# Kernel optimization log

Hardware: AMD Instinct MI355X
Metric: run time of the kernel (lower is better)

Reference implementation:

```python
import jax, jax.numpy as jnp
import numpy as np

B, T, C, H = 8, 2048, 1024, 64


def setup_inputs() -> dict:
    key = jax.random.key(0)
    k1, k2, k3, k4 = jax.random.split(key, 4)
    data = jax.random.normal(k1, (B, T, C), dtype=jnp.float32)
    # nn.Linear(embed, head, bias=False) weights, stored as [embed, head] so y = x @ W
    scale = C ** -0.5  # init-scale so activations stay O(1)
    Wq = jax.random.normal(k2, (C, H), dtype=jnp.float32) * scale
    Wk = jax.random.normal(k3, (C, H), dtype=jnp.float32) * scale
    Wv = jax.random.normal(k4, (C, H), dtype=jnp.float32) * scale
    return {"data": data, "Wq": Wq, "Wk": Wk, "Wv": Wv}


def reference(data, Wq, Wk, Wv):
    # data: [B, T, C]; self-attention (crossData=None), causal mask, eval-mode dropout.
    Bs, Ts, Cs = data.shape
    q = data @ Wq  # [B, T, H]
    k = data @ Wk  # [B, T, H]
    v = data @ Wv  # [B, T, H]
    # NOTE: original scales by C**-0.5 with C = embed_size (faithful to source).
    wei = jnp.einsum('btd,bsd->bts', q, k) * (Cs ** -0.5)  # [B, T, T]
    causal = jnp.tril(jnp.ones((Ts, Ts), dtype=bool))
    wei = jnp.where(causal[None, :, :], wei, -jnp.inf)
    wei = jax.nn.softmax(wei, axis=-1)
    out = jnp.einsum('bts,bsh->bth', wei, v)  # [B, T, H]
    return out
```

## Files before the change

### kernel.cpp

```cpp
#include <hip/hip_runtime.h>
#include <hip/hip_bf16.h>


typedef __bf16 bf16;
typedef __bf16 bf16x8 __attribute__((ext_vector_type(8)));
typedef float f32x4 __attribute__((ext_vector_type(4)));
typedef unsigned int u32;
typedef u32 u32x2 __attribute__((ext_vector_type(2)));
typedef u32 u32x4 __attribute__((ext_vector_type(4)));

#define T_SZ 2048
#define C_SZ 1024
#define H_SZ 64
#define QOFF 0
#define KOFF 1024
#define VOFF 2048
#define PPITCH 72
#define APITCH 1032
#define NEG_BIG (-30000.0f)
#define QSCALE 0.04508422f

__device__ __forceinline__ bf16x8 ld8(const bf16* p) { return *(const bf16x8*)p; }

template <int CTRL>
__device__ __forceinline__ float dpp_mov(float x) {
  return __builtin_bit_cast(float,
      __builtin_amdgcn_update_dpp(0, __builtin_bit_cast(int, x), CTRL, 0xf, 0xf, true));
}
__device__ __forceinline__ float qmax16(float x) {
  x = fmaxf(x, dpp_mov<0x121>(x));
  x = fmaxf(x, dpp_mov<0x122>(x));
  x = fmaxf(x, dpp_mov<0x124>(x));
  x = fmaxf(x, dpp_mov<0x128>(x));
  return x;
}
__device__ __forceinline__ float qsum16(float x) {
  x += dpp_mov<0x121>(x);
  x += dpp_mov<0x122>(x);
  x += dpp_mov<0x124>(x);
  x += dpp_mov<0x128>(x);
  return x;
}

__global__ __launch_bounds__(256) void transpose_w(const float* __restrict__ Wq,
                                                   const float* __restrict__ Wk,
                                                   const float* __restrict__ Wv,
                                                   bf16* __restrict__ Wt) {
  __shared__ float sh[64][65];
  int ct = blockIdx.x;
  int mat = blockIdx.y;
  const float* W = (mat == 0) ? Wq : (mat == 1 ? Wk : Wv);
  int tid = threadIdx.x;
  int r = tid >> 2, cb = (tid & 3) * 16;

  const f32x4* src = (const f32x4*)(W + (size_t)(ct * 64 + r) * H_SZ + cb);
#pragma unroll
  for (int v = 0; v < 4; ++v) {
    f32x4 x = src[v];
#pragma unroll
    for (int j = 0; j < 4; ++j) sh[r][cb + v * 4 + j] = x[j];
  }
  __syncthreads();

  float scale = (mat == 0) ? QSCALE : 1.0f;
  bf16x8 o0, o1;
#pragma unroll
  for (int j = 0; j < 8; ++j) o0[j] = (bf16)(sh[cb + j][r] * scale);
#pragma unroll
  for (int j = 0; j < 8; ++j) o1[j] = (bf16)(sh[cb + 8 + j][r] * scale);
  bf16* dst = Wt + ((size_t)mat * H_SZ + r) * C_SZ + ct * 64 + cb;
  *(bf16x8*)dst = o0;
  *(bf16x8*)(dst + 8) = o1;
}

__global__ __launch_bounds__(768, 3) void qkv(const float* data, const bf16* __restrict__ Wt,
                                              bf16* arena, int regsz) {
  __shared__ bf16 As[64 * 1024];
  char* As_b = (char*)As;
  int blk = blockIdx.x;
  int tid = threadIdx.x;
  int w = tid >> 6, lane = tid & 63;
  int l15 = lane & 15, quad = lane >> 4;

  const float* src = data + (size_t)blk * 64 * C_SZ;
#pragma unroll
  for (int g = 0; g < 3; ++g) {
    f32x4 st[7];
#pragma unroll
    for (int i = 0; i < 7; ++i) {
      int u = (g * 7 + i) * 768 + tid;
      st[i] = __builtin_nontemporal_load(
          (const f32x4*)(src + (size_t)(u >> 8) * C_SZ + (u & 255) * 4));
    }
#pragma unroll
    for (int i = 0; i < 7; ++i) {
      int u = (g * 7 + i) * 768 + tid;
      int row = u >> 8, c4 = u & 255;
      bf16 t4[4] = {(bf16)st[i][0], (bf16)st[i][1], (bf16)st[i][2], (bf16)st[i][3]};
      int bo = (row * 2048 + c4 * 8) ^ ((row & 7) << 4);
      *(u32x2*)(As_b + bo) = *(const u32x2*)t4;
    }
  }
  if (tid < 256) {
    int c4 = tid;
    f32x4 x = __builtin_nontemporal_load(
        (const f32x4*)(src + (size_t)63 * C_SZ + c4 * 4));
    bf16 t4[4] = {(bf16)x[0], (bf16)x[1], (bf16)x[2], (bf16)x[3]};
    int bo = (63 * 2048 + c4 * 8) ^ ((63 & 7) << 4);
    *(u32x2*)(As_b + bo) = *(const u32x2*)t4;
  }
  __syncthreads();

  int j = w;
  const bf16* wb = Wt + (size_t)(j * 16 + l15) * C_SZ + quad * 8;
  bf16x8 wf[2];
  wf[0] = ld8(wb);
  wf[1] = ld8(wb + 32);

  f32x4 acc[4];
  f32x4 zero = {0.f, 0.f, 0.f, 0.f};
#pragma unroll
  for (int rg = 0; rg < 4; ++rg) acc[rg] = zero;

  bool isQK = (j < 8);
  int swz = (l15 & 7) << 4;

#pragma unroll 2
  for (int kci = 0; kci < 32; ++kci) {
    int cur = kci & 1;
    bf16x8 df[4];
#pragma unroll
    for (int rg = 0; rg < 4; ++rg) {
      int bo = ((rg * 16 + l15) * 2048 + kci * 64 + quad * 16) ^ swz;
      df[rg] = ld8((const bf16*)(As_b + bo));
    }
    if (isQK) {
#pragma unroll
      for (int rg = 0; rg < 4; ++rg)
        acc[rg] = __builtin_amdgcn_mfma_f32_16x16x32_bf16(wf[cur], df[rg], acc[rg], 0, 0, 0);
    } else {
#pragma unroll
      for (int rg = 0; rg < 4; ++rg)
        acc[rg] = __builtin_amdgcn_mfma_f32_16x16x32_bf16(df[rg], wf[cur], acc[rg], 0, 0, 0);
    }
    wf[cur] = ld8(wb + ((kci + 2) & 31) * 32);
  }

#pragma unroll
  for (int rg = 0; rg < 4; ++rg) {
    bf16* reg = arena + (size_t)(blk * 4 + rg) * (size_t)regsz;
    bf16 p4[4] = {(bf16)acc[rg][0], (bf16)acc[rg][1], (bf16)acc[rg][2], (bf16)acc[rg][3]};
    if (j < 4) {
      bf16* dst = reg + QOFF + l15 * 64 + j * 16 + quad * 4;
      *(u32x2*)dst = *(const u32x2*)p4;
    } else if (j < 8) {
      bf16* dst = reg + KOFF + l15 * 64 + (j - 4) * 16 + quad * 4;
      *(u32x2*)dst = *(const u32x2*)p4;
    } else {
      bf16* dst = reg + VOFF + ((j - 8) * 16 + l15) * 16 + quad * 4;
      *(u32x2*)dst = *(const u32x2*)p4;
    }
  }
}

__global__ __launch_bounds__(256, 4) void attn(const bf16* __restrict__ arena,
                                               float* __restrict__ out, int regsz) {
  __shared__ bf16 Ps[4][16 * PPITCH];
  __shared__ f32x4 Mg[3][6][64];
  int id = blockIdx.x;
  int b = id & 7;
  int t = id >> 3;
  int slice = t & 3;
  int qt = 31 - (t >> 2);
  int tid = threadIdx.x;
  int w = tid >> 6, lane = tid & 63;
  int l15 = lane & 15, quad = lane >> 4;

  const bf16* base = arena + (size_t)b * 128 * (size_t)regsz;

  const bf16* qreg = base + (size_t)(qt * 4 + slice) * (size_t)regsz + QOFF + l15 * 64;
  bf16x8 qf0 = ld8(qreg + quad * 8);
  bf16x8 qf1 = ld8(qreg + 32 + quad * 8);

  f32x4 accO[4];
  f32x4 zero = {0.f, 0.f, 0.f, 0.f};
#pragma unroll
  for (int nt = 0; nt < 4; ++nt) accO[nt] = zero;
  float m[4], l[4];
#pragma unroll
  for (int r = 0; r < 4; ++r) { m[r] = NEG_BIG; l[r] = 0.f; }

  int qrow_base = qt * 64 + slice * 16 + quad * 4;
  int vro = (quad >> 1);
  int vco = (quad & 1) * 8;

  int q4 = (qt + 4) >> 2;
  int kbeg = w * q4;
  int kend = min((w + 1) * q4, qt + 1);

  for (int kt = kbeg; kt < kend; ++kt) {
    bf16x8 kf[8];
#pragma unroll
    for (int nt = 0; nt < 4; ++nt) {
      const bf16* kp = base + (size_t)(kt * 4 + nt) * (size_t)regsz + KOFF + l15 * 64 + quad * 8;
      kf[2 * nt] = ld8(kp);
      kf[2 * nt + 1] = ld8(kp + 32);
    }

    f32x4 sA[4];
#pragma unroll
    for (int nt = 0; nt < 4; ++nt) sA[nt] = zero;
#pragma unroll
    for (int nt = 0; nt < 4; ++nt) {
      sA[nt] = __builtin_amdgcn_mfma_f32_16x16x32_bf16(qf0, kf[2 * nt], sA[nt], 0, 0, 0);
      sA[nt] = __builtin_amdgcn_mfma_f32_16x16x32_bf16(qf1, kf[2 * nt + 1], sA[nt], 0, 0, 0);
    }

    bf16x8 vf0[4];
#pragma unroll
    for (int nt = 0; nt < 4; ++nt) {
      const bf16* vp = base + (size_t)(kt * 4 + vro) * (size_t)regsz + VOFF +
                       (nt * 16 + l15) * 16 + vco;
      vf0[nt] = ld8(vp);
    }

    if (kt == qt) {
#pragma unroll
      for (int nt = 0; nt < 4; ++nt) {
        int colg = kt * 64 + nt * 16 + l15;
#pragma unroll
        for (int r = 0; r < 4; ++r)
          if (colg > qrow_base + r) sA[nt][r] = NEG_BIG;
      }
    }

    float alpha[4];
#pragma unroll
    for (int r = 0; r < 4; ++r) {
      float mx = qmax16(fmaxf(fmaxf(sA[0][r], sA[1][r]), fmaxf(sA[2][r], sA[3][r])));
      float mnew = fmaxf(m[r], mx);
      alpha[r] = exp2f(m[r] - mnew);
      m[r] = mnew;
    }

    float rs[4] = {0.f, 0.f, 0.f, 0.f};
#pragma unroll
    for (int nt = 0; nt < 4; ++nt) {
#pragma unroll
      for (int r = 0; r < 4; ++r) {
        float p = exp2f(sA[nt][r] - m[r]);
        sA[nt][r] = p;
        rs[r] += p;
      }
    }
#pragma unroll
    for (int r = 0; r < 4; ++r) l[r] = l[r] * alpha[r] + qsum16(rs[r]);

#pragma unroll
    for (int nt = 0; nt < 4; ++nt) {
#pragma unroll
      for (int r = 0; r < 4; ++r)
        Ps[w][(quad * 4 + r) * PPITCH + nt * 16 + l15] = (bf16)sA[nt][r];
    }

    bf16x8 vf1[4];
#pragma unroll
    for (int nt = 0; nt < 4; ++nt) {
      const bf16* vp = base + (size_t)(kt * 4 + 2 + vro) * (size_t)regsz + VOFF +
                       (nt * 16 + l15) * 16 + vco;
      vf1[nt] = ld8(vp);
    }

#pragma unroll
    for (int nt = 0; nt < 4; ++nt) {
#pragma unroll
      for (int r = 0; r < 4; ++r) accO[nt][r] *= alpha[r];
    }
    bf16x8 pf0 = ld8((const bf16*)Ps[w] + l15 * PPITCH + quad * 8);
    bf16x8 pf1 = ld8((const bf16*)Ps[w] + l15 * PPITCH + 32 + quad * 8);
#pragma unroll
    for (int nt = 0; nt < 4; ++nt)
      accO[nt] = __builtin_amdgcn_mfma_f32_16x16x32_bf16(pf0, vf0[nt], accO[nt], 0, 0, 0);
#pragma unroll
    for (int nt = 0; nt < 4; ++nt)
      accO[nt] = __builtin_amdgcn_mfma_f32_16x16x32_bf16(pf1, vf1[nt], accO[nt], 0, 0, 0);
  }

  if (w > 0) {
#pragma unroll
    for (int nt = 0; nt < 4; ++nt) Mg[w - 1][nt][lane] = accO[nt];
    f32x4 mv = {m[0], m[1], m[2], m[3]};
    f32x4 lv = {l[0], l[1], l[2], l[3]};
    Mg[w - 1][4][lane] = mv;
    Mg[w - 1][5][lane] = lv;
  }
  __syncthreads();
  if (w == 0) {
#pragma unroll
    for (int wv = 0; wv < 3; ++wv) {
      f32x4 mo = Mg[wv][4][lane];
      f32x4 lo = Mg[wv][5][lane];
      f32x4 oo[4];
#pragma unroll
      for (int nt = 0; nt < 4; ++nt) oo[nt] = Mg[wv][nt][lane];
#pragma unroll
      for (int r = 0; r < 4; ++r) {
        float mnew = fmaxf(m[r], mo[r]);
        float a = exp2f(m[r] - mnew);
        float bs = exp2f(mo[r] - mnew);
        l[r] = l[r] * a + lo[r] * bs;
#pragma unroll
        for (int nt = 0; nt < 4; ++nt) accO[nt][r] = accO[nt][r] * a + oo[nt][r] * bs;
        m[r] = mnew;
      }
    }

    float inv[4];
#pragma unroll
    for (int r = 0; r < 4; ++r) inv[r] = 1.f / l[r];
#pragma unroll
    for (int nt = 0; nt < 4; ++nt) {
#pragma unroll
      for (int r = 0; r < 4; ++r) {
        int tk = qt * 64 + slice * 16 + quad * 4 + r;
        int h = nt * 16 + l15;
        out[((size_t)b * T_SZ + tk) * H_SZ + h] = accO[nt][r] * inv[r];
      }
    }
  }
}

extern "C" void kernel_launch(void* const* d_in, const int* in_sizes, int n_in,
                              void* d_out, int out_size, void* d_ws, size_t ws_size,
                              hipStream_t stream) {
  const float* data = (const float*)d_in[0];

  const size_t arena_bytes = (size_t)1024 * 4096 * sizeof(bf16);
  const size_t wt_bytes = (size_t)3 * H_SZ * C_SZ * sizeof(bf16);
  bool ws_ok = (d_ws != nullptr) && (ws_size >= arena_bytes + wt_bytes);

  bf16* arena = ws_ok ? (bf16*)d_ws : (bf16*)d_in[0];
  bf16* Wt = ws_ok ? (bf16*)((char*)d_ws + arena_bytes) : (bf16*)d_out;
  int regsz = ws_ok ? 4096 : 32768;

  transpose_w<<<dim3(16, 3), 256, 0, stream>>>((const float*)d_in[1],
                                               (const float*)d_in[2],
                                               (const float*)d_in[3], Wt);
  qkv<<<256, 768, 0, stream>>>(data, Wt, arena, regsz);
  attn<<<1024, 256, 0, stream>>>(arena, (float*)d_out, regsz);
}
```

Before: 143.2 us.

## Split QKV projection into two row halves to overlap global loads with MFMA

The qkv kernel now stages the 64-row data tile in two halves of 32 rows. Global loads for the second half are issued into registers before the MFMA loop over the first half, then converted and written to shared memory afterwards. The aim is to hide part of the global-load latency of the fp32 input behind compute. In exchange it holds more live registers (st2 is 11 x f32x4), which risks spills or lower occupancy under launch bounds of 768 threads and 3 blocks. It also streams the weight fragments twice, once per half.

Result: slower. 154.1 us (+7.6%).

```diff
diff --git a/kernel.cpp b/kernel.cpp
--- a/kernel.cpp
+++ b/kernel.cpp
@@ -16,7 +16,6 @@
 #define KOFF 1024
 #define VOFF 2048
 #define PPITCH 72
-#define APITCH 1032
 #define NEG_BIG (-30000.0f)
 #define QSCALE 0.04508422f
 
@@ -83,33 +82,40 @@
   int l15 = lane & 15, quad = lane >> 4;
 
   const float* src = data + (size_t)blk * 64 * C_SZ;
-#pragma unroll
-  for (int g = 0; g < 3; ++g) {
-    f32x4 st[7];
-#pragma unroll
-    for (int i = 0; i < 7; ++i) {
-      int u = (g * 7 + i) * 768 + tid;
-      st[i] = __builtin_nontemporal_load(
+
+  {
+    f32x4 st[11];
+#pragma unroll
+    for (int i = 0; i < 11; ++i) {
+      if (i < 10 || tid < 512) {
+        int u = i * 768 + tid;
+        st[i] = __builtin_nontemporal_load(
+            (const f32x4*)(src + (size_t)(u >> 8) * C_SZ + (u & 255) * 4));
+      }
+    }
+#pragma unroll
+    for (int i = 0; i < 11; ++i) {
+      if (i < 10 || tid < 512) {
+        int u = i * 768 + tid;
+        int row = u >> 8, c4 = u & 255;
+        bf16 t4[4] = {(bf16)st[i][0], (bf16)st[i][1], (bf16)st[i][2], (bf16)st[i][3]};
+        int bo = (row * 2048 + c4 * 8) ^ ((row & 7) << 4);
+        *(u32x2*)(As_b + bo) = *(const u32x2*)t4;
+      }
+    }
+  }
+  __syncthreads();
+
+  f32x4 st2[11];
+#pragma unroll
+  for (int i = 0; i < 11; ++i) {
+    if (i < 10 || tid < 512) {
+      int u = 8192 + i * 768 + tid;
+      st2[i] = __builtin_nontemporal_load(
           (const f32x4*)(src + (size_t)(u >> 8) * C_SZ + (u & 255) * 4));
     }
-#pragma unroll
-    for (int i = 0; i < 7; ++i) {
-      int u = (g * 7 + i) * 768 + tid;
-      int row = u >> 8, c4 = u & 255;
-      bf16 t4[4] = {(bf16)st[i][0], (bf16)st[i][1], (bf16)st[i][2], (bf16)st[i][3]};
-      int bo = (row * 2048 + c4 * 8) ^ ((row & 7) << 4);
-      *(u32x2*)(As_b + bo) = *(const u32x2*)t4;
-    }
-  }
-  if (tid < 256) {
-    int c4 = tid;
-    f32x4 x = __builtin_nontemporal_load(
-        (const f32x4*)(src + (size_t)63 * C_SZ + c4 * 4));
-    bf16 t4[4] = {(bf16)x[0], (bf16)x[1], (bf16)x[2], (bf16)x[3]};
-    int bo = (63 * 2048 + c4 * 8) ^ ((63 & 7) << 4);
-    *(u32x2*)(As_b + bo) = *(const u32x2*)t4;
-  }
-  __syncthreads();
+  }
+  __builtin_amdgcn_sched_barrier(0);
 
   int j = w;
   const bf16* wb = Wt + (size_t)(j * 16 + l15) * C_SZ + quad * 8;
@@ -128,20 +134,49 @@
 #pragma unroll 2
   for (int kci = 0; kci < 32; ++kci) {
     int cur = kci & 1;
-    bf16x8 df[4];
-#pragma unroll
-    for (int rg = 0; rg < 4; ++rg) {
+    bf16x8 df[2];
+#pragma unroll
+    for (int rg = 0; rg < 2; ++rg) {
       int bo = ((rg * 16 + l15) * 2048 + kci * 64 + quad * 16) ^ swz;
       df[rg] = ld8((const bf16*)(As_b + bo));
     }
     if (isQK) {
-#pragma unroll
-      for (int rg = 0; rg < 4; ++rg)
-        acc[rg] = __builtin_amdgcn_mfma_f32_16x16x32_bf16(wf[cur], df[rg], acc[rg], 0, 0, 0);
+      acc[0] = __builtin_amdgcn_mfma_f32_16x16x32_bf16(wf[cur], df[0], acc[0], 0, 0, 0);
+      acc[1] = __builtin_amdgcn_mfma_f32_16x16x32_bf16(wf[cur], df[1], acc[1], 0, 0, 0);
     } else {
-#pragma unroll
-      for (int rg = 0; rg < 4; ++rg)
-        acc[rg] = __builtin_amdgcn_mfma_f32_16x16x32_bf16(df[rg], wf[cur], acc[rg], 0, 0, 0);
+      acc[0] = __builtin_amdgcn_mfma_f32_16x16x32_bf16(df[0], wf[cur], acc[0], 0, 0, 0);
+      acc[1] = __builtin_amdgcn_mfma_f32_16x16x32_bf16(df[1], wf[cur], acc[1], 0, 0, 0);
+    }
+    wf[cur] = ld8(wb + ((kci + 2) & 31) * 32);
+  }
+
+#pragma unroll
+  for (int i = 0; i < 11; ++i) {
+    if (i < 10 || tid < 512) {
+      int u = 8192 + i * 768 + tid;
+      int row = u >> 8, c4 = u & 255;
+      bf16 t4[4] = {(bf16)st2[i][0], (bf16)st2[i][1], (bf16)st2[i][2], (bf16)st2[i][3]};
+      int bo = (row * 2048 + c4 * 8) ^ ((row & 7) << 4);
+      *(u32x2*)(As_b + bo) = *(const u32x2*)t4;
+    }
+  }
+  __syncthreads();
+
+#pragma unroll 2
+  for (int kci = 0; kci < 32; ++kci) {
+    int cur = kci & 1;
+    bf16x8 df[2];
+#pragma unroll
+    for (int rg = 0; rg < 2; ++rg) {
+      int bo = (((rg + 2) * 16 + l15) * 2048 + kci * 64 + quad * 16) ^ swz;
+      df[rg] = ld8((const bf16*)(As_b + bo));
+    }
+    if (isQK) {
+      acc[2] = __builtin_amdgcn_mfma_f32_16x16x32_bf16(wf[cur], df[0], acc[2], 0, 0, 0);
+      acc[3] = __builtin_amdgcn_mfma_f32_16x16x32_bf16(wf[cur], df[1], acc[3], 0, 0, 0);
+    } else {
+      acc[2] = __builtin_amdgcn_mfma_f32_16x16x32_bf16(df[0], wf[cur], acc[2], 0, 0, 0);
+      acc[3] = __builtin_amdgcn_mfma_f32_16x16x32_bf16(df[1], wf[cur], acc[3], 0, 0, 0);
     }
     wf[cur] = ld8(wb + ((kci + 2) & 31) * 32);
   }
```
